# Performance work log

Hardware: AMD Instinct MI355X
Metric: run time of the kernel (lower is better)

Reference implementation:

```python
import jax, jax.numpy as jnp
import numpy as np

N_NODES = 100_000
N_EDGES = 1_600_000
IN_FEAT = 128
N_HEADS = 8
OUT_FEAT = 16
HF = N_HEADS * OUT_FEAT  # 128
NEG_SLOPE = 0.2


def setup_inputs() -> dict:
    key = jax.random.key(0)
    k = jax.random.split(key, 9)
    x = jax.random.normal(k[0], (N_NODES, IN_FEAT), dtype=jnp.float32)
    src = jax.random.randint(k[1], (N_EDGES,), 0, N_NODES, dtype=jnp.int64)
    dst = jax.random.randint(k[2], (N_EDGES,), 0, N_NODES, dtype=jnp.int64)
    sv = 1.0 / np.sqrt(IN_FEAT)
    sa = 1.0 / np.sqrt(HF)
    Wv = jax.random.normal(k[3], (IN_FEAT, HF), dtype=jnp.float32) * sv
    bv = jnp.zeros((HF,), dtype=jnp.float32)
    Wq = jax.random.normal(k[4], (HF, N_HEADS), dtype=jnp.float32) * sa
    bq = jnp.zeros((N_HEADS,), dtype=jnp.float32)
    Wk = jax.random.normal(k[5], (HF, N_HEADS), dtype=jnp.float32) * sa
    bk = jnp.zeros((N_HEADS,), dtype=jnp.float32)
    return {"x": x, "src": src, "dst": dst, "Wv": Wv, "bv": bv,
            "Wq": Wq, "bq": bq, "Wk": Wk, "bk": bk}


def reference(x, src, dst, Wv, bv, Wq, bq, Wk, bk):
    # Dense projections (homogeneous graph: h_src == h_dst == h)
    h = x @ Wv + bv                       # [N, H*F]
    q = h @ Wq + bq                       # [N, H]  (query, attached via dst)
    k = h @ Wk + bk                       # [N, H]  (key, attached via src)
    u = h.reshape(N_NODES, N_HEADS, OUT_FEAT)  # [N, H, F]

    # Edge scores: u_add_v('k','q') -> e_ij = k[src] + q[dst], then leaky-relu
    e = k[src] + q[dst]                   # [E, H]
    coeff = jnp.where(e >= 0, e, NEG_SLOPE * e)

    # Segment softmax over incoming edges of each destination node
    seg_max = jax.ops.segment_max(coeff, dst, num_segments=N_NODES)   # [N, H]
    ex = jnp.exp(coeff - seg_max[dst])                                # [E, H]
    denom = jax.ops.segment_sum(ex, dst, num_segments=N_NODES)       # [N, H]
    attn = ex / denom[dst]                                           # [E, H]

    # Weighted message + scatter-sum aggregate
    m = u[src] * attn[:, :, None]                                    # [E, H, F]
    v = jax.ops.segment_sum(m, dst, num_segments=N_NODES)            # [N, H, F]

    return jnp.mean(v, axis=1)                                       # [N, F]
```

## Files before the change

kernel.cpp:

```cpp
#include <hip/hip_runtime.h>
#include <hip/hip_fp16.h>

#define NFEAT 128
#define NHEADS 8
#define OUTF 16
#define NPB 256
#define MAXNB 512
#define CAP 4736

typedef _Float16 half8 __attribute__((ext_vector_type(8)));
typedef float float4v __attribute__((ext_vector_type(4)));

__global__ __launch_bounds__(256) void prep_kernel(
    const float* __restrict__ Wv, const float* __restrict__ bv,
    const float* __restrict__ Wq, const float* __restrict__ bq,
    const float* __restrict__ Wk, const float* __restrict__ bk,
    float* __restrict__ Wvq, float* __restrict__ Wvk,
    float* __restrict__ bq2, float* __restrict__ bk2)
{
    const int t = threadIdx.x;
    const int idx = blockIdx.x * 256 + t;
    const int m  = idx >> 10;
    const int j  = (idx >> 3) & 127;
    const int hd = idx & 7;
    const float* w = m ? Wk : Wq;
    float acc = 0.f;
#pragma unroll 8
    for (int c = 0; c < NFEAT; c++) acc += Wv[j * NFEAT + c] * w[c * NHEADS + hd];
    if (m) Wvk[j * NHEADS + hd] = acc;
    else   Wvq[j * NHEADS + hd] = acc;

    if (blockIdx.x == 0 && t < 16) {
        int mm = t >> 3, hh = t & 7;
        const float* ww = mm ? Wk : Wq;
        float a = mm ? bk[hh] : bq[hh];
        for (int c = 0; c < NFEAT; c++) a += bv[c] * ww[c * NHEADS + hh];
        if (mm) bk2[hh] = a;
        else    bq2[hh] = a;
    }
}

__global__ __launch_bounds__(256) void gemm_h_kernel(
    const float* __restrict__ x, const float* __restrict__ Wv,
    const float* __restrict__ bv, const float* __restrict__ Wvq,
    const float* __restrict__ Wvk, const float* __restrict__ bq2,
    const float* __restrict__ bk2, __half* __restrict__ h,
    float* __restrict__ qarr, float* __restrict__ karr, int M)
{
    __shared__ _Float16 sw[144][136];
    const int t = threadIdx.x;

    for (int i = t; i < 128 * 128; i += 256) {
        int k = i >> 7, n = i & 127;
        sw[n][k] = (_Float16)Wv[i];
    }
    for (int i = t; i < 128 * 16; i += 256) {
        int k = i >> 4, o = i & 15;
        float v = (o < 8) ? Wvq[k * 8 + o] : Wvk[k * 8 + (o - 8)];
        sw[128 + o][k] = (_Float16)v;
    }
    __syncthreads();

    const int wave = t >> 6, lane = t & 63;
    const int quad = lane >> 4, l16 = lane & 15;
    const int nstrips = (M + 15) >> 4;

    float bvv[8];
#pragma unroll
    for (int tl = 0; tl < 8; tl++) bvv[tl] = bv[tl * 16 + l16];
    const float qb = (l16 < 8) ? bq2[l16] : bk2[l16 - 8];

#pragma unroll
    for (int s = 0; s < 2; s++) {
        const int strip = blockIdx.x * 8 + wave + s * 4;
        if (strip >= nstrips) break;
        const int row0 = strip * 16;
        const int xr = row0 + l16;
        const bool ok = (xr < M);
        const float* xp = x + (size_t)xr * NFEAT + quad * 8;

        half8 af[4];
#pragma unroll
        for (int kc = 0; kc < 4; kc++) {
            float4 f0 = make_float4(0.f, 0.f, 0.f, 0.f);
            float4 f1 = make_float4(0.f, 0.f, 0.f, 0.f);
            if (ok) {
                f0 = *(const float4*)(xp + kc * 32);
                f1 = *(const float4*)(xp + kc * 32 + 4);
            }
            half8 a;
            a[0] = (_Float16)f0.x; a[1] = (_Float16)f0.y;
            a[2] = (_Float16)f0.z; a[3] = (_Float16)f0.w;
            a[4] = (_Float16)f1.x; a[5] = (_Float16)f1.y;
            a[6] = (_Float16)f1.z; a[7] = (_Float16)f1.w;
            af[kc] = a;
        }

        float4v acc[9];
#pragma unroll
        for (int tl = 0; tl < 9; tl++) acc[tl] = (float4v){0.f, 0.f, 0.f, 0.f};

#pragma unroll
        for (int kc = 0; kc < 4; kc++) {
#pragma unroll
            for (int tl = 0; tl < 9; tl++) {
                half8 b = *(const half8*)&sw[tl * 16 + l16][kc * 32 + quad * 8];
                acc[tl] = __builtin_amdgcn_mfma_f32_16x16x32_f16(af[kc], b, acc[tl], 0, 0, 0);
            }
        }

#pragma unroll
        for (int r = 0; r < 4; r++) {
            int row = row0 + quad * 4 + r;
            if (row < M) {
#pragma unroll
                for (int tl = 0; tl < 8; tl++)
                    h[(size_t)row * NFEAT + tl * 16 + l16] =
                        __float2half(acc[tl][r] + bvv[tl]);
                float qv = acc[8][r] + qb;
                if (l16 < 8) qarr[(size_t)row * NHEADS + l16] = qv;
                else         karr[(size_t)row * NHEADS + (l16 - 8)] = qv;
            }
        }
    }
}

__global__ __launch_bounds__(1024) void bin_kernel(
    const int* __restrict__ src, const int* __restrict__ dst,
    int* __restrict__ tail, int* __restrict__ bin, int E, int NB)
{
    __shared__ int lcnt[MAXNB];
    __shared__ int lbase[MAXNB];
    const int t = threadIdx.x;
    const int e0 = blockIdx.x * 8192;

    for (int i = t; i < NB; i += 1024) lcnt[i] = 0;
    __syncthreads();

    int pack[8], bkt[8], rank[8];
#pragma unroll
    for (int k = 0; k < 8; k++) {
        int e = e0 + k * 1024 + t;
        bkt[k] = -1;
        if (e < E) {
            int d = dst[e];
            pack[k] = (src[e] << 8) | (d & (NPB - 1));
            bkt[k]  = d >> 8;
            rank[k] = atomicAdd(&lcnt[bkt[k]], 1);
        }
    }
    __syncthreads();
    for (int i = t; i < NB; i += 1024)
        lbase[i] = lcnt[i] ? atomicAdd(&tail[i], lcnt[i]) : 0;
    __syncthreads();

#pragma unroll
    for (int k = 0; k < 8; k++) {
        if (bkt[k] >= 0) {
            int pos = lbase[bkt[k]] + rank[k];
            if (pos < CAP) bin[(size_t)bkt[k] * CAP + pos] = pack[k];
        }
    }
}

__global__ __launch_bounds__(1024) void bucket_build_kernel(
    const int* __restrict__ bin, const int* __restrict__ tail,
    int* __restrict__ deg, int* __restrict__ off,
    int* __restrict__ csr, int N, int NB)
{
    __shared__ int stail[MAXNB];
    __shared__ int lcnt[NPB];
    __shared__ int lcur[NPB];
    __shared__ int lcsr[CAP];

    const int b = blockIdx.x;
    const int t = threadIdx.x;

    for (int i = t; i < MAXNB; i += 1024) stail[i] = (i < NB) ? tail[i] : 0;
    if (t < NPB) lcnt[t] = 0;
    __syncthreads();

    for (int o = 1; o < MAXNB; o <<= 1) {
        int u = (t < MAXNB && t >= o) ? stail[t - o] : 0;
        __syncthreads();
        if (t < MAXNB) stail[t] += u;
        __syncthreads();
    }
    const int gbase = (b > 0) ? stail[b - 1] : 0;
    const int cnt = min(tail[b], CAP);
    const int n0 = b << 8;
    const int* mybin = bin + (size_t)b * CAP;

    for (int i = t; i < cnt; i += 1024) atomicAdd(&lcnt[mybin[i] & (NPB - 1)], 1);
    __syncthreads();

    if (t < NPB) lcur[t] = lcnt[t];
    __syncthreads();
    for (int o = 1; o < NPB; o <<= 1) {
        int u = (t < NPB && t >= o) ? lcur[t - o] : 0;
        __syncthreads();
        if (t < NPB) lcur[t] += u;
        __syncthreads();
    }
    if (t < NPB) {
        int excl = lcur[t] - lcnt[t];
        lcur[t] = excl;
        int node = n0 + t;
        if (node < N) {
            deg[node] = lcnt[t];
            off[node] = gbase + excl;
        }
    }
    __syncthreads();

    for (int i = t; i < cnt; i += 1024) {
        int p = mybin[i];
        int r = atomicAdd(&lcur[p & (NPB - 1)], 1);
        lcsr[r] = p >> 8;
    }
    __syncthreads();

    for (int i = t; i < cnt; i += 1024) csr[gbase + i] = lcsr[i];
}

__global__ __launch_bounds__(256) void agg_kernel(
    const int* __restrict__ csr, const int* __restrict__ off,
    const int* __restrict__ deg, const float* __restrict__ karr,
    const float* __restrict__ qarr, const __half* __restrict__ h,
    float* __restrict__ out, int nnodes)
{
    const int wave = threadIdx.x >> 6;
    const int lane = threadIdx.x & 63;
    const int d = blockIdx.x * 4 + wave;
    if (d >= nnodes) return;

    const int dg = deg[d];
    const int o0 = off[d];
    const int h8  = lane & 7;
    const int eg  = lane >> 4;
    const int l16 = lane & 15;
    const int hd  = l16 >> 1;
    const float q1 = qarr[d * NHEADS + h8];
    const __half* hbase = h + l16 * 8;

    __half2 acc0 = __float2half2_rn(0.f);
    __half2 acc1 = __float2half2_rn(0.f);
    __half2 acc2 = __float2half2_rn(0.f);
    __half2 acc3 = __float2half2_rn(0.f);
    float den8 = 0.f;

    for (int c0 = 0; c0 < dg; c0 += 64) {
        const int cnt = min(64, dg - c0);
        int sv = (lane < cnt) ? csr[o0 + c0 + lane] : 0;
        for (int g0 = 0; g0 < cnt; g0 += 8) {
            const int epos = g0 + (lane >> 3);
            int s8 = __shfl(sv, epos, 64);
            float p = 0.f;
            if (epos < cnt) {
                float c = karr[s8 * NHEADS + h8] + q1;
                c = fmaxf(c, 0.2f * c);
                p = __expf(c) * 0.0009765625f;
            }
            den8 += p;
            __half2 ph2 = __half2half2(__float2half(p));
            int phi = *(int*)&ph2;
#pragma unroll
            for (int i = 0; i < 2; ++i) {
                int jr  = (i << 2) + eg;
                int sl  = __shfl(sv, g0 + jr, 64);
                int pw  = __shfl(phi, (jr << 3) + hd, 64);
                __half2 pv = *(__half2*)&pw;
                float4 raw = *(const float4*)(hbase + (size_t)sl * NFEAT);
                __half2 v0 = *(__half2*)&raw.x;
                __half2 v1 = *(__half2*)&raw.y;
                __half2 v2 = *(__half2*)&raw.z;
                __half2 v3 = *(__half2*)&raw.w;
                acc0 = __hfma2(pv, v0, acc0);
                acc1 = __hfma2(pv, v1, acc1);
                acc2 = __hfma2(pv, v2, acc2);
                acc3 = __hfma2(pv, v3, acc3);
            }
        }
    }

    den8 += __shfl_xor(den8, 8, 64);
    den8 += __shfl_xor(den8, 16, 64);
    den8 += __shfl_xor(den8, 32, 64);
    float dh = __shfl(den8, hd, 64);

    float f[8];
    f[0] = __low2float(acc0); f[1] = __high2float(acc0);
    f[2] = __low2float(acc1); f[3] = __high2float(acc1);
    f[4] = __low2float(acc2); f[5] = __high2float(acc2);
    f[6] = __low2float(acc3); f[7] = __high2float(acc3);

#pragma unroll
    for (int o = 16; o <= 32; o <<= 1)
#pragma unroll
        for (int i = 0; i < 8; i++) f[i] += __shfl_xor(f[i], o, 64);

    const float inv = (dg > 0) ? 0.125f / dh : 0.f;
#pragma unroll
    for (int i = 0; i < 8; i++) f[i] *= inv;

#pragma unroll
    for (int o = 2; o <= 8; o <<= 1)
#pragma unroll
        for (int i = 0; i < 8; i++) f[i] += __shfl_xor(f[i], o, 64);

    if (lane < 2) {
        float4* o4 = (float4*)(out + (size_t)d * OUTF + lane * 8);
        o4[0] = make_float4(f[0], f[1], f[2], f[3]);
        o4[1] = make_float4(f[4], f[5], f[6], f[7]);
    }
}

extern "C" void kernel_launch(void* const* d_in, const int* in_sizes, int n_in,
                              void* d_out, int out_size, void* d_ws, size_t ws_size,
                              hipStream_t stream)
{
    const float* x   = (const float*)d_in[0];
    const int*   src = (const int*)d_in[1];
    const int*   dst = (const int*)d_in[2];
    const float* Wv  = (const float*)d_in[3];
    const float* bv  = (const float*)d_in[4];
    const float* Wq  = (const float*)d_in[5];
    const float* bq  = (const float*)d_in[6];
    const float* Wk  = (const float*)d_in[7];
    const float* bk  = (const float*)d_in[8];
    float* out = (float*)d_out;

    const int N = in_sizes[0] / NFEAT;
    const int E = in_sizes[1];
    const int NB = (N + NPB - 1) / NPB;

    __half* h   = (__half*)d_ws;
    float* qarr = (float*)d_ws + (size_t)N * (NFEAT / 2);
    float* karr = qarr + (size_t)N * NHEADS;
    int* deg    = (int*)(karr + (size_t)N * NHEADS);
    int* off    = deg + N;
    int* csr    = off + N;
    float* Wvq  = (float*)(csr + E);
    float* Wvk  = Wvq + NFEAT * NHEADS;
    float* bq2  = Wvk + NFEAT * NHEADS;
    float* bk2  = bq2 + NHEADS;
    int* tail   = (int*)(bk2 + NHEADS);
    int* bin    = tail + MAXNB;

    hipMemsetAsync(tail, 0, MAXNB * sizeof(int), stream);

    prep_kernel<<<dim3(8), dim3(256), 0, stream>>>(Wv, bv, Wq, bq, Wk, bk,
                                                   Wvq, Wvk, bq2, bk2);

    bin_kernel<<<dim3((E + 8191) / 8192), dim3(1024), 0, stream>>>(
        src, dst, tail, bin, E, NB);

    bucket_build_kernel<<<dim3(NB), dim3(1024), 0, stream>>>(
        bin, tail, deg, off, csr, N, NB);

    const int nstrips = (N + 15) / 16;
    gemm_h_kernel<<<dim3((nstrips + 7) / 8), dim3(256), 0, stream>>>(
        x, Wv, bv, Wvq, Wvk, bq2, bk2, h, qarr, karr, N);

    agg_kernel<<<dim3((N + 3) / 4), dim3(256), 0, stream>>>(
        csr, off, deg, karr, qarr, h, out, N);
}
```

Baseline: 241.0 us.

## Assign one 16-lane group per destination node in aggregation kernel

The aggregation kernel now maps each destination node to a 16-thread group instead of a full 64-lane wave, with each lane owning 8 feature halves. Every group walks its edge list four edges at a time, issuing four independent row gathers and key loads per step and keeping four separate half2 accumulator sets. This removes the cross-lane shuffles used to broadcast source ids and probabilities, and it avoids idle lanes on low-degree nodes, since the average degree is about 16. In exchange, nodes with different degrees inside the same wave now diverge, and each lane holds more registers and recomputes exp redundantly for its head.

```diff
diff --git a/kernel.cpp b/kernel.cpp
--- a/kernel.cpp
+++ b/kernel.cpp
@@ -229,87 +229,95 @@
     const float* __restrict__ qarr, const __half* __restrict__ h,
     float* __restrict__ out, int nnodes)
 {
-    const int wave = threadIdx.x >> 6;
-    const int lane = threadIdx.x & 63;
-    const int d = blockIdx.x * 4 + wave;
+    const int g = threadIdx.x >> 4;
+    const int j = threadIdx.x & 15;
+    const int d = blockIdx.x * 16 + g;
     if (d >= nnodes) return;
 
     const int dg = deg[d];
     const int o0 = off[d];
-    const int h8  = lane & 7;
-    const int eg  = lane >> 4;
-    const int l16 = lane & 15;
-    const int hd  = l16 >> 1;
-    const float q1 = qarr[d * NHEADS + h8];
-    const __half* hbase = h + l16 * 8;
-
-    __half2 acc0 = __float2half2_rn(0.f);
-    __half2 acc1 = __float2half2_rn(0.f);
-    __half2 acc2 = __float2half2_rn(0.f);
-    __half2 acc3 = __float2half2_rn(0.f);
-    float den8 = 0.f;
-
-    for (int c0 = 0; c0 < dg; c0 += 64) {
-        const int cnt = min(64, dg - c0);
-        int sv = (lane < cnt) ? csr[o0 + c0 + lane] : 0;
-        for (int g0 = 0; g0 < cnt; g0 += 8) {
-            const int epos = g0 + (lane >> 3);
-            int s8 = __shfl(sv, epos, 64);
-            float p = 0.f;
-            if (epos < cnt) {
-                float c = karr[s8 * NHEADS + h8] + q1;
-                c = fmaxf(c, 0.2f * c);
-                p = __expf(c) * 0.0009765625f;
-            }
-            den8 += p;
-            __half2 ph2 = __half2half2(__float2half(p));
-            int phi = *(int*)&ph2;
-#pragma unroll
-            for (int i = 0; i < 2; ++i) {
-                int jr  = (i << 2) + eg;
-                int sl  = __shfl(sv, g0 + jr, 64);
-                int pw  = __shfl(phi, (jr << 3) + hd, 64);
-                __half2 pv = *(__half2*)&pw;
-                float4 raw = *(const float4*)(hbase + (size_t)sl * NFEAT);
-                __half2 v0 = *(__half2*)&raw.x;
-                __half2 v1 = *(__half2*)&raw.y;
-                __half2 v2 = *(__half2*)&raw.z;
-                __half2 v3 = *(__half2*)&raw.w;
-                acc0 = __hfma2(pv, v0, acc0);
-                acc1 = __hfma2(pv, v1, acc1);
-                acc2 = __hfma2(pv, v2, acc2);
-                acc3 = __hfma2(pv, v3, acc3);
-            }
-        }
-    }
-
-    den8 += __shfl_xor(den8, 8, 64);
-    den8 += __shfl_xor(den8, 16, 64);
-    den8 += __shfl_xor(den8, 32, 64);
-    float dh = __shfl(den8, hd, 64);
+    const int hd = j >> 1;
+    const float q1 = qarr[d * NHEADS + hd];
+    const __half* hbase = h + j * 8;
+
+    __half2 acc[4][4];
+#pragma unroll
+    for (int u = 0; u < 4; u++)
+#pragma unroll
+        for (int i = 0; i < 4; i++) acc[u][i] = __float2half2_rn(0.f);
+    float den = 0.f;
+
+    for (int e = 0; e < dg; e += 4) {
+        const int rem = dg - e;
+        const int s0 = csr[o0 + e];
+        const int s1 = (rem > 1) ? csr[o0 + e + 1] : s0;
+        const int s2 = (rem > 2) ? csr[o0 + e + 2] : s0;
+        const int s3 = (rem > 3) ? csr[o0 + e + 3] : s0;
+
+        const float4 r0 = *(const float4*)(hbase + (size_t)s0 * NFEAT);
+        const float4 r1 = *(const float4*)(hbase + (size_t)s1 * NFEAT);
+        const float4 r2 = *(const float4*)(hbase + (size_t)s2 * NFEAT);
+        const float4 r3 = *(const float4*)(hbase + (size_t)s3 * NFEAT);
+
+        float c0 = karr[s0 * NHEADS + hd] + q1;
+        float c1 = karr[s1 * NHEADS + hd] + q1;
+        float c2 = karr[s2 * NHEADS + hd] + q1;
+        float c3 = karr[s3 * NHEADS + hd] + q1;
+        c0 = fmaxf(c0, 0.2f * c0);
+        c1 = fmaxf(c1, 0.2f * c1);
+        c2 = fmaxf(c2, 0.2f * c2);
+        c3 = fmaxf(c3, 0.2f * c3);
+        const float p0 = __expf(c0) * 0.0009765625f;
+        const float p1 = (rem > 1) ? __expf(c1) * 0.0009765625f : 0.f;
+        const float p2 = (rem > 2) ? __expf(c2) * 0.0009765625f : 0.f;
+        const float p3 = (rem > 3) ? __expf(c3) * 0.0009765625f : 0.f;
+        den += (p0 + p1) + (p2 + p3);
+
+        const __half2 pv0 = __half2half2(__float2half(p0));
+        const __half2 pv1 = __half2half2(__float2half(p1));
+        const __half2 pv2 = __half2half2(__float2half(p2));
+        const __half2 pv3 = __half2half2(__float2half(p3));
+
+        acc[0][0] = __hfma2(pv0, *(const __half2*)&r0.x, acc[0][0]);
+        acc[0][1] = __hfma2(pv0, *(const __half2*)&r0.y, acc[0][1]);
+        acc[0][2] = __hfma2(pv0, *(const __half2*)&r0.z, acc[0][2]);
+        acc[0][3] = __hfma2(pv0, *(const __half2*)&r0.w, acc[0][3]);
+        acc[1][0] = __hfma2(pv1, *(const __half2*)&r1.x, acc[1][0]);
+        acc[1][1] = __hfma2(pv1, *(const __half2*)&r1.y, acc[1][1]);
+        acc[1][2] = __hfma2(pv1, *(const __half2*)&r1.z, acc[1][2]);
+        acc[1][3] = __hfma2(pv1, *(const __half2*)&r1.w, acc[1][3]);
+        acc[2][0] = __hfma2(pv2, *(const __half2*)&r2.x, acc[2][0]);
+        acc[2][1] = __hfma2(pv2, *(const __half2*)&r2.y, acc[2][1]);
+        acc[2][2] = __hfma2(pv2, *(const __half2*)&r2.z, acc[2][2]);
+        acc[2][3] = __hfma2(pv2, *(const __half2*)&r2.w, acc[2][3]);
+        acc[3][0] = __hfma2(pv3, *(const __half2*)&r3.x, acc[3][0]);
+        acc[3][1] = __hfma2(pv3, *(const __half2*)&r3.y, acc[3][1]);
+        acc[3][2] = __hfma2(pv3, *(const __half2*)&r3.z, acc[3][2]);
+        acc[3][3] = __hfma2(pv3, *(const __half2*)&r3.w, acc[3][3]);
+    }
 
     float f[8];
-    f[0] = __low2float(acc0); f[1] = __high2float(acc0);
-    f[2] = __low2float(acc1); f[3] = __high2float(acc1);
-    f[4] = __low2float(acc2); f[5] = __high2float(acc2);
-    f[6] = __low2float(acc3); f[7] = __high2float(acc3);
-
-#pragma unroll
-    for (int o = 16; o <= 32; o <<= 1)
+#pragma unroll
+    for (int i = 0; i < 4; i++) {
+        float2 t0 = __half22float2(acc[0][i]);
+        float2 t1 = __half22float2(acc[1][i]);
+        float2 t2 = __half22float2(acc[2][i]);
+        float2 t3 = __half22float2(acc[3][i]);
+        f[2 * i]     = (t0.x + t1.x) + (t2.x + t3.x);
+        f[2 * i + 1] = (t0.y + t1.y) + (t2.y + t3.y);
+    }
+
+    const float inv = (dg > 0) ? 0.125f / den : 0.f;
+#pragma unroll
+    for (int i = 0; i < 8; i++) f[i] *= inv;
+
+#pragma unroll
+    for (int o = 2; o <= 8; o <<= 1)
 #pragma unroll
         for (int i = 0; i < 8; i++) f[i] += __shfl_xor(f[i], o, 64);
 
-    const float inv = (dg > 0) ? 0.125f / dh : 0.f;
-#pragma unroll
-    for (int i = 0; i < 8; i++) f[i] *= inv;
-
-#pragma unroll
-    for (int o = 2; o <= 8; o <<= 1)
-#pragma unroll
-        for (int i = 0; i < 8; i++) f[i] += __shfl_xor(f[i], o, 64);
-
-    if (lane < 2) {
-        float4* o4 = (float4*)(out + (size_t)d * OUTF + lane * 8);
+    if (j < 2) {
+        float4* o4 = (float4*)(out + (size_t)d * OUTF + j * 8);
         o4[0] = make_float4(f[0], f[1], f[2], f[3]);
         o4[1] = make_float4(f[4], f[5], f[6], f[7]);
     }
@@ -362,6 +370,6 @@
     gemm_h_kernel<<<dim3((nstrips + 7) / 8), dim3(256), 0, stream>>>(
         x, Wv, bv, Wvq, Wvk, bq2, bk2, h, qarr, karr, N);
 
-    agg_kernel<<<dim3((N + 3) / 4), dim3(256), 0, stream>>>(
+    agg_kernel<<<dim3((N + 15) / 16), dim3(256), 0, stream>>>(
         csr, off, deg, karr, qarr, h, out, N);
 }
```

Result: no change. 237.3 us (-1.5%).

## Quantize node features to int8 with per-row scale and regroup aggregation lanes

Applied to the files above, without the earlier changes.

The GEMM epilogue now stores h as int8 with a per-node absmax scale instead of fp16, halving the bytes of the random row gathers in aggregation. The aggregation kernel is restructured so 8 lanes handle one destination node, one lane per head. Each lane gathers 16 int8 values per edge, 8 edges at a time, and accumulates in fp32. This trades gather bandwidth and cross-lane shuffles for int8-to-float unpack ALU work and lower precision in the features.

```diff
diff --git a/kernel.cpp b/kernel.cpp
--- a/kernel.cpp
+++ b/kernel.cpp
@@ -44,8 +44,9 @@
     const float* __restrict__ x, const float* __restrict__ Wv,
     const float* __restrict__ bv, const float* __restrict__ Wvq,
     const float* __restrict__ Wvk, const float* __restrict__ bq2,
-    const float* __restrict__ bk2, __half* __restrict__ h,
-    float* __restrict__ qarr, float* __restrict__ karr, int M)
+    const float* __restrict__ bk2, unsigned char* __restrict__ hq,
+    float* __restrict__ sarr, float* __restrict__ qarr,
+    float* __restrict__ karr, int M)
 {
     __shared__ _Float16 sw[144][136];
     const int t = threadIdx.x;
@@ -113,10 +114,23 @@
         for (int r = 0; r < 4; r++) {
             int row = row0 + quad * 4 + r;
             if (row < M) {
-#pragma unroll
-                for (int tl = 0; tl < 8; tl++)
-                    h[(size_t)row * NFEAT + tl * 16 + l16] =
-                        __float2half(acc[tl][r] + bvv[tl]);
+                float vv[8];
+                float mx = 0.f;
+#pragma unroll
+                for (int tl = 0; tl < 8; tl++) {
+                    vv[tl] = acc[tl][r] + bvv[tl];
+                    mx = fmaxf(mx, fabsf(vv[tl]));
+                }
+#pragma unroll
+                for (int o = 1; o <= 8; o <<= 1)
+                    mx = fmaxf(mx, __shfl_xor(mx, o, 64));
+                const float is = (mx > 0.f) ? 127.f / mx : 0.f;
+#pragma unroll
+                for (int tl = 0; tl < 8; tl++) {
+                    int qi = __float2int_rn(vv[tl] * is);
+                    hq[(size_t)row * NFEAT + tl * 16 + l16] = (unsigned char)(signed char)qi;
+                }
+                if (l16 == 0) sarr[row] = mx * (1.f / 127.f);
                 float qv = acc[8][r] + qb;
                 if (l16 < 8) qarr[(size_t)row * NHEADS + l16] = qv;
                 else         karr[(size_t)row * NHEADS + (l16 - 8)] = qv;
@@ -226,92 +240,85 @@
 __global__ __launch_bounds__(256) void agg_kernel(
     const int* __restrict__ csr, const int* __restrict__ off,
     const int* __restrict__ deg, const float* __restrict__ karr,
-    const float* __restrict__ qarr, const __half* __restrict__ h,
-    float* __restrict__ out, int nnodes)
-{
-    const int wave = threadIdx.x >> 6;
-    const int lane = threadIdx.x & 63;
-    const int d = blockIdx.x * 4 + wave;
+    const float* __restrict__ qarr, const unsigned char* __restrict__ hq,
+    const float* __restrict__ sarr, float* __restrict__ out, int nnodes)
+{
+    const int g = threadIdx.x >> 3;
+    const int j = threadIdx.x & 7;
+    const int d = blockIdx.x * 32 + g;
     if (d >= nnodes) return;
 
     const int dg = deg[d];
     const int o0 = off[d];
-    const int h8  = lane & 7;
-    const int eg  = lane >> 4;
-    const int l16 = lane & 15;
-    const int hd  = l16 >> 1;
-    const float q1 = qarr[d * NHEADS + h8];
-    const __half* hbase = h + l16 * 8;
-
-    __half2 acc0 = __float2half2_rn(0.f);
-    __half2 acc1 = __float2half2_rn(0.f);
-    __half2 acc2 = __float2half2_rn(0.f);
-    __half2 acc3 = __float2half2_rn(0.f);
-    float den8 = 0.f;
-
-    for (int c0 = 0; c0 < dg; c0 += 64) {
-        const int cnt = min(64, dg - c0);
-        int sv = (lane < cnt) ? csr[o0 + c0 + lane] : 0;
-        for (int g0 = 0; g0 < cnt; g0 += 8) {
-            const int epos = g0 + (lane >> 3);
-            int s8 = __shfl(sv, epos, 64);
-            float p = 0.f;
-            if (epos < cnt) {
-                float c = karr[s8 * NHEADS + h8] + q1;
-                c = fmaxf(c, 0.2f * c);
-                p = __expf(c) * 0.0009765625f;
-            }
-            den8 += p;
-            __half2 ph2 = __half2half2(__float2half(p));
-            int phi = *(int*)&ph2;
-#pragma unroll
-            for (int i = 0; i < 2; ++i) {
-                int jr  = (i << 2) + eg;
-                int sl  = __shfl(sv, g0 + jr, 64);
-                int pw  = __shfl(phi, (jr << 3) + hd, 64);
-                __half2 pv = *(__half2*)&pw;
-                float4 raw = *(const float4*)(hbase + (size_t)sl * NFEAT);
-                __half2 v0 = *(__half2*)&raw.x;
-                __half2 v1 = *(__half2*)&raw.y;
-                __half2 v2 = *(__half2*)&raw.z;
-                __half2 v3 = *(__half2*)&raw.w;
-                acc0 = __hfma2(pv, v0, acc0);
-                acc1 = __hfma2(pv, v1, acc1);
-                acc2 = __hfma2(pv, v2, acc2);
-                acc3 = __hfma2(pv, v3, acc3);
-            }
-        }
-    }
-
-    den8 += __shfl_xor(den8, 8, 64);
-    den8 += __shfl_xor(den8, 16, 64);
-    den8 += __shfl_xor(den8, 32, 64);
-    float dh = __shfl(den8, hd, 64);
-
-    float f[8];
-    f[0] = __low2float(acc0); f[1] = __high2float(acc0);
-    f[2] = __low2float(acc1); f[3] = __high2float(acc1);
-    f[4] = __low2float(acc2); f[5] = __high2float(acc2);
-    f[6] = __low2float(acc3); f[7] = __high2float(acc3);
-
-#pragma unroll
-    for (int o = 16; o <= 32; o <<= 1)
-#pragma unroll
-        for (int i = 0; i < 8; i++) f[i] += __shfl_xor(f[i], o, 64);
-
-    const float inv = (dg > 0) ? 0.125f / dh : 0.f;
-#pragma unroll
-    for (int i = 0; i < 8; i++) f[i] *= inv;
-
-#pragma unroll
-    for (int o = 2; o <= 8; o <<= 1)
-#pragma unroll
-        for (int i = 0; i < 8; i++) f[i] += __shfl_xor(f[i], o, 64);
-
-    if (lane < 2) {
-        float4* o4 = (float4*)(out + (size_t)d * OUTF + lane * 8);
-        o4[0] = make_float4(f[0], f[1], f[2], f[3]);
-        o4[1] = make_float4(f[4], f[5], f[6], f[7]);
+    const float q1 = qarr[d * NHEADS + j];
+    const unsigned char* hb = hq + j * 16;
+
+    float acc[16];
+#pragma unroll
+    for (int i = 0; i < 16; i++) acc[i] = 0.f;
+    float den = 0.f;
+
+    for (int e = 0; e < dg; e += 8) {
+        const int rem = dg - e;
+        int s[8];
+        s[0] = csr[o0 + e];
+#pragma unroll
+        for (int k = 1; k < 8; k++) s[k] = (rem > k) ? csr[o0 + e + k] : s[0];
+
+        int4  r[8];
+        float kv[8];
+        float sc[8];
+#pragma unroll
+        for (int k = 0; k < 8; k++) {
+            r[k]  = *(const int4*)(hb + (size_t)s[k] * NFEAT);
+            kv[k] = karr[s[k] * NHEADS + j];
+            sc[k] = sarr[s[k]];
+        }
+
+#pragma unroll
+        for (int k = 0; k < 8; k++) {
+            float c = kv[k] + q1;
+            c = fmaxf(c, 0.2f * c);
+            const float p = (rem > k) ? __expf(c) * 0.0009765625f : 0.f;
+            den += p;
+            const float w = p * sc[k];
+            const int4 rv = r[k];
+            const int d0 = rv.x, d1 = rv.y, d2 = rv.z, d3 = rv.w;
+            acc[0]  = fmaf(w, (float)(signed char)(d0      ), acc[0]);
+            acc[1]  = fmaf(w, (float)(signed char)(d0 >>  8), acc[1]);
+            acc[2]  = fmaf(w, (float)(signed char)(d0 >> 16), acc[2]);
+            acc[3]  = fmaf(w, (float)(d0 >> 24),              acc[3]);
+            acc[4]  = fmaf(w, (float)(signed char)(d1      ), acc[4]);
+            acc[5]  = fmaf(w, (float)(signed char)(d1 >>  8), acc[5]);
+            acc[6]  = fmaf(w, (float)(signed char)(d1 >> 16), acc[6]);
+            acc[7]  = fmaf(w, (float)(d1 >> 24),              acc[7]);
+            acc[8]  = fmaf(w, (float)(signed char)(d2      ), acc[8]);
+            acc[9]  = fmaf(w, (float)(signed char)(d2 >>  8), acc[9]);
+            acc[10] = fmaf(w, (float)(signed char)(d2 >> 16), acc[10]);
+            acc[11] = fmaf(w, (float)(d2 >> 24),              acc[11]);
+            acc[12] = fmaf(w, (float)(signed char)(d3      ), acc[12]);
+            acc[13] = fmaf(w, (float)(signed char)(d3 >>  8), acc[13]);
+            acc[14] = fmaf(w, (float)(signed char)(d3 >> 16), acc[14]);
+            acc[15] = fmaf(w, (float)(d3 >> 24),              acc[15]);
+        }
+    }
+
+    const float inv = (dg > 0) ? 0.125f / den : 0.f;
+    float f[16];
+#pragma unroll
+    for (int i = 0; i < 16; i++) f[i] = acc[i] * inv;
+
+#pragma unroll
+    for (int o = 1; o <= 4; o <<= 1)
+#pragma unroll
+        for (int i = 0; i < 16; i++) f[i] += __shfl_xor(f[i], o, 64);
+
+    if (j == 0) {
+        float4* o4 = (float4*)(out + (size_t)d * OUTF);
+        o4[0] = make_float4(f[0],  f[1],  f[2],  f[3]);
+        o4[1] = make_float4(f[4],  f[5],  f[6],  f[7]);
+        o4[2] = make_float4(f[8],  f[9],  f[10], f[11]);
+        o4[3] = make_float4(f[12], f[13], f[14], f[15]);
     }
 }
 
@@ -334,8 +341,9 @@
     const int E = in_sizes[1];
     const int NB = (N + NPB - 1) / NPB;
 
-    __half* h   = (__half*)d_ws;
-    float* qarr = (float*)d_ws + (size_t)N * (NFEAT / 2);
+    unsigned char* hq = (unsigned char*)d_ws;
+    float* sarr = (float*)(hq + (size_t)N * NFEAT);
+    float* qarr = sarr + N;
     float* karr = qarr + (size_t)N * NHEADS;
     int* deg    = (int*)(karr + (size_t)N * NHEADS);
     int* off    = deg + N;
@@ -360,8 +368,8 @@
 
     const int nstrips = (N + 15) / 16;
     gemm_h_kernel<<<dim3((nstrips + 7) / 8), dim3(256), 0, stream>>>(
-        x, Wv, bv, Wvq, Wvk, bq2, bk2, h, qarr, karr, N);
-
-    agg_kernel<<<dim3((N + 3) / 4), dim3(256), 0, stream>>>(
-        csr, off, deg, karr, qarr, h, out, N);
-}
+        x, Wv, bv, Wvq, Wvk, bq2, bk2, hq, sarr, qarr, karr, N);
+
+    agg_kernel<<<dim3((N + 31) / 32), dim3(256), 0, stream>>>(
+        csr, off, deg, karr, qarr, hq, sarr, out, N);
+}
```

Result: faster. 211.3 us (-12.3%).
